# Kernel optimization log

Measured on AMD Instinct MI355X. Metric: run time of the kernel, lower is better.

The kernel has to match this reference:

```python
import jax, jax.numpy as jnp
import numpy as np

N_NODES = 100_000
N_EDGES = 1_600_000
F_NODE = 128
F_EDGE = 128
HIDDEN = 256
OUT = 128


def setup_inputs() -> dict:
    key = jax.random.key(0)
    k = jax.random.split(key, 7)
    x = jax.random.normal(k[0], (N_NODES, F_NODE), dtype=jnp.float32)
    edge_index = jax.random.randint(k[1], (2, N_EDGES), 0, N_NODES, dtype=jnp.int64)
    edge_attr = jax.random.normal(k[2], (N_EDGES, F_EDGE), dtype=jnp.float32)
    fan_in1 = F_NODE + F_EDGE
    W1 = jax.random.normal(k[3], (HIDDEN, fan_in1), dtype=jnp.float32) / np.sqrt(fan_in1)
    b1 = jnp.zeros((HIDDEN,), dtype=jnp.float32)
    W2 = jax.random.normal(k[4], (OUT, HIDDEN), dtype=jnp.float32) / np.sqrt(HIDDEN)
    b2 = jnp.zeros((OUT,), dtype=jnp.float32)
    return {"x": x, "edge_index": edge_index, "edge_attr": edge_attr,
            "W1": W1, "b1": b1, "W2": W2, "b2": b2}


def reference(x, edge_index, edge_attr, W1, b1, W2, b2):
    col = edge_index[1]
    # scatter-mean of edge_attr into target nodes (dim_size = #nodes)
    summed = jax.ops.segment_sum(edge_attr, col, num_segments=N_NODES)  # [N, F_edge]
    counts = jax.ops.segment_sum(jnp.ones((edge_attr.shape[0],), dtype=edge_attr.dtype),
                                 col, num_segments=N_NODES)
    agg = summed / jnp.maximum(counts, 1.0)[:, None]
    h = jnp.concatenate([x, agg], axis=1)          # [N, F_node + F_edge]
    h = jax.nn.relu(h @ W1.T + b1)                 # hidden Linear + ReLU
    return h @ W2.T + b2                           # final linear layer
```

## Files before the change

kernel.cpp:

```cpp
#include <hip/hip_runtime.h>
#include <hip/hip_bf16.h>
#include <stdint.h>

#define N_NODES 100000
#define N_EDGES 1600000
#define F_NODE 128
#define F_EDGE 128
#define HIDDEN 256
#define OUT_F 128
#define K_DIM 256
#define CAP 64

using f32x4 = __attribute__((ext_vector_type(4))) float;
using s16x8 = __attribute__((ext_vector_type(8))) short;

typedef __attribute__((address_space(3))) unsigned lds_u32;
typedef __attribute__((address_space(1))) const unsigned gbl_u32;

static __device__ __forceinline__ short f2b(float f) {
  union { float f; unsigned u; } v; v.f = f;
  unsigned r = v.u + 0x7fffu + ((v.u >> 16) & 1u);
  return (short)(r >> 16);
}
static __device__ __forceinline__ void gld_lds16(const void* g, void* l) {
  __builtin_amdgcn_global_load_lds((gbl_u32*)g, (lds_u32*)l, 16, 0, 0);
}


__global__ void k_fill(const int* __restrict__ col,
                       unsigned* __restrict__ cursor,
                       unsigned* __restrict__ ids) {
  int e = blockIdx.x * blockDim.x + threadIdx.x;
  if (e < N_EDGES) {
    int n = col[e];
    unsigned slot = atomicAdd(&cursor[n], 1u);
    if (slot < CAP) ids[(size_t)n * CAP + slot] = (unsigned)e;
  }
}


__global__ void k_cvt2(const float* __restrict__ W1, const float* __restrict__ W2,
                       short* __restrict__ w1b, short* __restrict__ w2b) {
  int i = (blockIdx.x * blockDim.x + threadIdx.x) * 4;
  if (i < HIDDEN * K_DIM) {
    f32x4 v = *reinterpret_cast<const f32x4*>(W1 + i);
    short4 s; s.x = f2b(v[0]); s.y = f2b(v[1]); s.z = f2b(v[2]); s.w = f2b(v[3]);
    *reinterpret_cast<short4*>(w1b + i) = s;
  } else {
    int j = i - HIDDEN * K_DIM;
    if (j < OUT_F * HIDDEN) {
      f32x4 v = *reinterpret_cast<const f32x4*>(W2 + j);
      short4 s; s.x = f2b(v[0]); s.y = f2b(v[1]); s.z = f2b(v[2]); s.w = f2b(v[3]);
      *reinterpret_cast<short4*>(w2b + j) = s;
    }
  }
}


__global__ void k_agg(const float* __restrict__ x,
                      const float* __restrict__ edge_attr,
                      const unsigned* __restrict__ cursor,
                      const unsigned* __restrict__ ids,
                      short* __restrict__ hin) {
  int n = (int)((blockIdx.x * (unsigned)blockDim.x + threadIdx.x) >> 6);
  int lane = threadIdx.x & 63;
  if (n >= N_NODES) return;
  int half = lane >> 5, l32 = lane & 31;
  unsigned cnt = cursor[n]; cnt = cnt > CAP ? CAP : cnt;
  const unsigned* idp = ids + (size_t)n * CAP;
  f32x4 a = {0.f, 0.f, 0.f, 0.f};
  const float* eb = edge_attr + 4 * l32;
  unsigned i = 0;
  for (; i + 8 <= cnt; i += 8) {
    unsigned e0 = idp[i + 0 + half];
    unsigned e1 = idp[i + 2 + half];
    unsigned e2 = idp[i + 4 + half];
    unsigned e3 = idp[i + 6 + half];
    f32x4 v0 = *reinterpret_cast<const f32x4*>(eb + (size_t)e0 * F_EDGE);
    f32x4 v1 = *reinterpret_cast<const f32x4*>(eb + (size_t)e1 * F_EDGE);
    f32x4 v2 = *reinterpret_cast<const f32x4*>(eb + (size_t)e2 * F_EDGE);
    f32x4 v3 = *reinterpret_cast<const f32x4*>(eb + (size_t)e3 * F_EDGE);
    a += v0 + v1 + v2 + v3;
  }
  for (; i + 2 <= cnt; i += 2) {
    unsigned e = idp[i + half];
    a += *reinterpret_cast<const f32x4*>(eb + (size_t)e * F_EDGE);
  }
  if (i < cnt && half == 0) {
    unsigned e = idp[i];
    a += *reinterpret_cast<const f32x4*>(eb + (size_t)e * F_EDGE);
  }
  f32x4 bsw;
  bsw[0] = __shfl_xor(a[0], 32); bsw[1] = __shfl_xor(a[1], 32);
  bsw[2] = __shfl_xor(a[2], 32); bsw[3] = __shfl_xor(a[3], 32);
  a += bsw;
  float inv = 1.0f / (float)(cnt > 0u ? cnt : 1u);
  float2 xv = *reinterpret_cast<const float2*>(x + (size_t)n * F_NODE + 2 * lane);
  short2 hx; hx.x = f2b(xv.x); hx.y = f2b(xv.y);
  short* hrow = hin + (size_t)n * K_DIM;
  *reinterpret_cast<short2*>(hrow + 2 * lane) = hx;
  if (half == 0) {
    short4 hm;
    hm.x = f2b(a[0] * inv); hm.y = f2b(a[1] * inv);
    hm.z = f2b(a[2] * inv); hm.w = f2b(a[3] * inv);
    *reinterpret_cast<short4*>(hrow + F_NODE + 4 * l32) = hm;
  }
}


__global__ __launch_bounds__(512) void k_mlp(const short* __restrict__ A,
                                             const short* __restrict__ W1b,
                                             const float* __restrict__ b1,
                                             const short* __restrict__ W2b,
                                             const float* __restrict__ b2,
                                             float* __restrict__ out, int M) {
  __shared__ short lds[128 * 256];
  const int t = threadIdx.x;
  const int lane = t & 63, wid = t >> 6;
  const int mrow0 = blockIdx.x * 128;
  const int lr = lane & 15;
  const int lkb = (lane >> 4) << 4;

  char* ldsb = (char*)lds;
#pragma unroll
  for (int j = 0; j < 8; ++j) {
    int chunk = j * 512 + t;
    int row = chunk >> 5;
    int kb = (chunk & 31) << 4;
    int src_kb = kb ^ ((row & 15) << 5);
    int grow = mrow0 + row; grow = grow < M ? grow : M - 1;
    const char* gsrc = (const char*)A + (size_t)grow * 512 + src_kb;
    char* ldst = ldsb + (size_t)(j * 512 + wid * 64) * 16;
    gld_lds16(gsrc, ldst);
  }
  __syncthreads();

  const int wr = wid >> 2;
  const int wc = wid & 3;
  f32x4 acc1[4][4] = {};
  for (int ksb = 0; ksb < 512; ksb += 64) {
    s16x8 af[4], bf[4];
#pragma unroll
    for (int m = 0; m < 4; ++m) {
      int row = wr * 64 + m * 16 + lr;
      int kb = (ksb + lkb) ^ ((row & 15) << 5);
      af[m] = *reinterpret_cast<const s16x8*>(ldsb + row * 512 + kb);
    }
#pragma unroll
    for (int nn = 0; nn < 4; ++nn) {
      int c = wc * 64 + nn * 16 + lr;
      bf[nn] = *reinterpret_cast<const s16x8*>(W1b + (size_t)c * 256 + ((ksb + lkb) >> 1));
    }
#pragma unroll
    for (int m = 0; m < 4; ++m)
#pragma unroll
      for (int nn = 0; nn < 4; ++nn)
        acc1[m][nn] = __builtin_amdgcn_mfma_f32_16x16x32_bf16(af[m], bf[nn], acc1[m][nn], 0, 0, 0);
  }
  __syncthreads();

#pragma unroll
  for (int nn = 0; nn < 4; ++nn) {
    int c = wc * 64 + nn * 16 + lr;
    float bv = b1[c];
#pragma unroll
    for (int m = 0; m < 4; ++m) {
#pragma unroll
      for (int j = 0; j < 4; ++j) {
        int r = wr * 64 + m * 16 + (lane >> 4) * 4 + j;
        float v = acc1[m][nn][j] + bv;
        v = v > 0.f ? v : 0.f;
        *reinterpret_cast<short*>(ldsb + r * 512 + ((c * 2) ^ ((r & 15) << 5))) = f2b(v);
      }
    }
  }
  __syncthreads();

  const int wr2 = wid >> 1;
  const int wc2 = wid & 1;
  f32x4 acc2[2][4] = {};
  for (int ksb = 0; ksb < 512; ksb += 64) {
    s16x8 af[2], bf[4];
#pragma unroll
    for (int m = 0; m < 2; ++m) {
      int row = wr2 * 32 + m * 16 + lr;
      int kb = (ksb + lkb) ^ ((row & 15) << 5);
      af[m] = *reinterpret_cast<const s16x8*>(ldsb + row * 512 + kb);
    }
#pragma unroll
    for (int nn = 0; nn < 4; ++nn) {
      int c = wc2 * 64 + nn * 16 + lr;
      bf[nn] = *reinterpret_cast<const s16x8*>(W2b + (size_t)c * 256 + ((ksb + lkb) >> 1));
    }
#pragma unroll
    for (int m = 0; m < 2; ++m)
#pragma unroll
      for (int nn = 0; nn < 4; ++nn)
        acc2[m][nn] = __builtin_amdgcn_mfma_f32_16x16x32_bf16(af[m], bf[nn], acc2[m][nn], 0, 0, 0);
  }
#pragma unroll
  for (int nn = 0; nn < 4; ++nn) {
    int c = wc2 * 64 + nn * 16 + lr;
    float bv = b2[c];
#pragma unroll
    for (int m = 0; m < 2; ++m) {
#pragma unroll
      for (int j = 0; j < 4; ++j) {
        int r = mrow0 + wr2 * 32 + m * 16 + (lane >> 4) * 4 + j;
        if (r < M) out[(size_t)r * OUT_F + c] = acc2[m][nn][j] + bv;
      }
    }
  }
}


extern "C" void kernel_launch(void* const* d_in, const int* in_sizes, int n_in,
                              void* d_out, int out_size, void* d_ws, size_t ws_size,
                              hipStream_t stream) {
  const float* x         = (const float*)d_in[0];
  const int*   edge_idx  = (const int*)d_in[1];
  const int*   col       = edge_idx + N_EDGES;
  const float* edge_attr = (const float*)d_in[2];
  const float* W1        = (const float*)d_in[3];
  const float* b1        = (const float*)d_in[4];
  const float* W2        = (const float*)d_in[5];
  const float* b2        = (const float*)d_in[6];
  float* out = (float*)d_out;

  char* ws = (char*)d_ws;
  unsigned* cursor = (unsigned*)(ws + 0);
  unsigned* ids    = (unsigned*)(ws + 400000);
  short*    hin    = (short*)   (ws + 26000000);
  short*    w1b    = (short*)   (ws + 77200000);
  short*    w2b    = (short*)   (ws + 77331072);

  hipMemsetAsync(cursor, 0, 400000, stream);

  k_cvt2<<<(HIDDEN * K_DIM + OUT_F * HIDDEN) / 4 / 256, 256, 0, stream>>>(W1, W2, w1b, w2b);
  k_fill<<<(N_EDGES + 255) / 256, 256, 0, stream>>>(col, cursor, ids);
  k_agg <<<(N_NODES * 64 + 255) / 256, 256, 0, stream>>>(x, edge_attr, cursor, ids, hin);
  k_mlp <<<(N_NODES + 127) / 128, 512, 0, stream>>>(hin, w1b, b1, w2b, b2, out, N_NODES);
}
```

Measured before the change: 433.2 us.

## Halve MLP row tile, merge fill and weight-convert kernels, bound agg occupancy

```diff
diff --git a/kernel.cpp b/kernel.cpp
--- a/kernel.cpp
+++ b/kernel.cpp
@@ -11,6 +11,9 @@
 #define K_DIM 256
 #define CAP 64
 
+#define FILL_BLOCKS ((N_EDGES + 255) / 256)
+#define CVT_BLOCKS  ((HIDDEN * K_DIM + OUT_F * HIDDEN) / 4 / 256)
+
 using f32x4 = __attribute__((ext_vector_type(4))) float;
 using s16x8 = __attribute__((ext_vector_type(8))) short;
 
@@ -27,41 +30,44 @@
 }
 
 
-__global__ void k_fill(const int* __restrict__ col,
-                       unsigned* __restrict__ cursor,
-                       unsigned* __restrict__ ids) {
-  int e = blockIdx.x * blockDim.x + threadIdx.x;
-  if (e < N_EDGES) {
-    int n = col[e];
-    unsigned slot = atomicAdd(&cursor[n], 1u);
-    if (slot < CAP) ids[(size_t)n * CAP + slot] = (unsigned)e;
-  }
-}
-
-
-__global__ void k_cvt2(const float* __restrict__ W1, const float* __restrict__ W2,
-                       short* __restrict__ w1b, short* __restrict__ w2b) {
-  int i = (blockIdx.x * blockDim.x + threadIdx.x) * 4;
-  if (i < HIDDEN * K_DIM) {
-    f32x4 v = *reinterpret_cast<const f32x4*>(W1 + i);
-    short4 s; s.x = f2b(v[0]); s.y = f2b(v[1]); s.z = f2b(v[2]); s.w = f2b(v[3]);
-    *reinterpret_cast<short4*>(w1b + i) = s;
+__global__ void k_fill_cvt(const int* __restrict__ col,
+                           unsigned* __restrict__ cursor,
+                           unsigned* __restrict__ ids,
+                           const float* __restrict__ W1,
+                           const float* __restrict__ W2,
+                           short* __restrict__ w1b,
+                           short* __restrict__ w2b) {
+  int bid = blockIdx.x;
+  if (bid < FILL_BLOCKS) {
+    int e = bid * 256 + threadIdx.x;
+    if (e < N_EDGES) {
+      int n = col[e];
+      unsigned slot = atomicAdd(&cursor[n], 1u);
+      if (slot < CAP) ids[(size_t)n * CAP + slot] = (unsigned)e;
+    }
   } else {
-    int j = i - HIDDEN * K_DIM;
-    if (j < OUT_F * HIDDEN) {
-      f32x4 v = *reinterpret_cast<const f32x4*>(W2 + j);
+    int i = ((bid - FILL_BLOCKS) * 256 + threadIdx.x) * 4;
+    if (i < HIDDEN * K_DIM) {
+      f32x4 v = *reinterpret_cast<const f32x4*>(W1 + i);
       short4 s; s.x = f2b(v[0]); s.y = f2b(v[1]); s.z = f2b(v[2]); s.w = f2b(v[3]);
-      *reinterpret_cast<short4*>(w2b + j) = s;
-    }
-  }
-}
-
-
-__global__ void k_agg(const float* __restrict__ x,
-                      const float* __restrict__ edge_attr,
-                      const unsigned* __restrict__ cursor,
-                      const unsigned* __restrict__ ids,
-                      short* __restrict__ hin) {
+      *reinterpret_cast<short4*>(w1b + i) = s;
+    } else {
+      int j = i - HIDDEN * K_DIM;
+      if (j < OUT_F * HIDDEN) {
+        f32x4 v = *reinterpret_cast<const f32x4*>(W2 + j);
+        short4 s; s.x = f2b(v[0]); s.y = f2b(v[1]); s.z = f2b(v[2]); s.w = f2b(v[3]);
+        *reinterpret_cast<short4*>(w2b + j) = s;
+      }
+    }
+  }
+}
+
+
+__global__ __launch_bounds__(256, 8) void k_agg(const float* __restrict__ x,
+                                                const float* __restrict__ edge_attr,
+                                                const unsigned* __restrict__ cursor,
+                                                const unsigned* __restrict__ ids,
+                                                short* __restrict__ hin) {
   int n = (int)((blockIdx.x * (unsigned)blockDim.x + threadIdx.x) >> 6);
   int lane = threadIdx.x & 63;
   if (n >= N_NODES) return;
@@ -80,7 +86,7 @@
     f32x4 v1 = *reinterpret_cast<const f32x4*>(eb + (size_t)e1 * F_EDGE);
     f32x4 v2 = *reinterpret_cast<const f32x4*>(eb + (size_t)e2 * F_EDGE);
     f32x4 v3 = *reinterpret_cast<const f32x4*>(eb + (size_t)e3 * F_EDGE);
-    a += v0 + v1 + v2 + v3;
+    a += (v0 + v1) + (v2 + v3);
   }
   for (; i + 2 <= cnt; i += 2) {
     unsigned e = idp[i + half];
@@ -108,41 +114,40 @@
 }
 
 
-__global__ __launch_bounds__(512) void k_mlp(const short* __restrict__ A,
+__global__ __launch_bounds__(256) void k_mlp(const short* __restrict__ A,
                                              const short* __restrict__ W1b,
                                              const float* __restrict__ b1,
                                              const short* __restrict__ W2b,
                                              const float* __restrict__ b2,
                                              float* __restrict__ out, int M) {
-  __shared__ short lds[128 * 256];
+  __shared__ short lds[64 * 256];
   const int t = threadIdx.x;
   const int lane = t & 63, wid = t >> 6;
-  const int mrow0 = blockIdx.x * 128;
+  const int mrow0 = blockIdx.x * 64;
   const int lr = lane & 15;
   const int lkb = (lane >> 4) << 4;
-
   char* ldsb = (char*)lds;
+
 #pragma unroll
   for (int j = 0; j < 8; ++j) {
-    int chunk = j * 512 + t;
+    int chunk = j * 256 + t;
     int row = chunk >> 5;
     int kb = (chunk & 31) << 4;
     int src_kb = kb ^ ((row & 15) << 5);
     int grow = mrow0 + row; grow = grow < M ? grow : M - 1;
     const char* gsrc = (const char*)A + (size_t)grow * 512 + src_kb;
-    char* ldst = ldsb + (size_t)(j * 512 + wid * 64) * 16;
+    char* ldst = ldsb + (size_t)(j * 256 + wid * 64) * 16;
     gld_lds16(gsrc, ldst);
   }
   __syncthreads();
 
-  const int wr = wid >> 2;
-  const int wc = wid & 3;
+  const int wc = wid;
   f32x4 acc1[4][4] = {};
   for (int ksb = 0; ksb < 512; ksb += 64) {
     s16x8 af[4], bf[4];
 #pragma unroll
     for (int m = 0; m < 4; ++m) {
-      int row = wr * 64 + m * 16 + lr;
+      int row = m * 16 + lr;
       int kb = (ksb + lkb) ^ ((row & 15) << 5);
       af[m] = *reinterpret_cast<const s16x8*>(ldsb + row * 512 + kb);
     }
@@ -167,7 +172,7 @@
     for (int m = 0; m < 4; ++m) {
 #pragma unroll
       for (int j = 0; j < 4; ++j) {
-        int r = wr * 64 + m * 16 + (lane >> 4) * 4 + j;
+        int r = m * 16 + (lane >> 4) * 4 + j;
         float v = acc1[m][nn][j] + bv;
         v = v > 0.f ? v : 0.f;
         *reinterpret_cast<short*>(ldsb + r * 512 + ((c * 2) ^ ((r & 15) << 5))) = f2b(v);
@@ -236,8 +241,8 @@
 
   hipMemsetAsync(cursor, 0, 400000, stream);
 
-  k_cvt2<<<(HIDDEN * K_DIM + OUT_F * HIDDEN) / 4 / 256, 256, 0, stream>>>(W1, W2, w1b, w2b);
-  k_fill<<<(N_EDGES + 255) / 256, 256, 0, stream>>>(col, cursor, ids);
-  k_agg <<<(N_NODES * 64 + 255) / 256, 256, 0, stream>>>(x, edge_attr, cursor, ids, hin);
-  k_mlp <<<(N_NODES + 127) / 128, 512, 0, stream>>>(hin, w1b, b1, w2b, b2, out, N_NODES);
-}
+  k_fill_cvt<<<FILL_BLOCKS + CVT_BLOCKS, 256, 0, stream>>>(col, cursor, ids,
+                                                           W1, W2, w1b, w2b);
+  k_agg<<<(N_NODES * 64 + 255) / 256, 256, 0, stream>>>(x, edge_attr, cursor, ids, hin);
+  k_mlp<<<(N_NODES + 63) / 64, 256, 0, stream>>>(hin, w1b, b1, w2b, b2, out, N_NODES);
+}
```

New measurement: 411.8 us. 1.05x faster.
